# Kernel optimization log

Measured on AMD Instinct MI355X. Metric: run time of the kernel, lower is better.

The kernel has to match this reference:

```python
import jax, jax.numpy as jnp
import numpy as np
from jax import lax

B, S, T = 512, 64, 32
E, H = 512, 1024
VIN, VOUT = 128, 128


def gru_cell(x, h, W_ih, W_hh, b_ih, b_hh):
    # PyTorch GRU cell: gates ordered (r, z, n)
    gi = x @ W_ih.T + b_ih           # [B, 3*Hh]
    gh = h @ W_hh.T + b_hh           # [B, 3*Hh]
    i_r, i_z, i_n = jnp.split(gi, 3, axis=-1)
    h_r, h_z, h_n = jnp.split(gh, 3, axis=-1)
    r = jax.nn.sigmoid(i_r + h_r)
    z = jax.nn.sigmoid(i_z + h_z)
    n = jnp.tanh(i_n + r * h_n)
    return (1.0 - z) * n + z * h


def setup_inputs() -> dict:
    key = jax.random.key(0)
    ks = jax.random.split(key, 18)
    g = lambda k, shp: (jax.random.normal(k, shp, jnp.float32) * 0.05)
    return {
        "src": jax.random.randint(ks[0], (B, S), 0, VIN),
        "tgt": jax.random.randint(ks[1], (B, T), 0, VOUT),
        "enc_emb": g(ks[2], (VIN, E)),
        "dec_emb": g(ks[3], (VOUT, E)),
        "W_ih_f": g(ks[4], (3 * H, E)), "W_hh_f": g(ks[5], (3 * H, H)),
        "b_ih_f": g(ks[6], (3 * H,)), "b_hh_f": g(ks[7], (3 * H,)),
        "W_ih_b": g(ks[8], (3 * H, E)), "W_hh_b": g(ks[9], (3 * H, H)),
        "b_ih_b": g(ks[10], (3 * H,)), "b_hh_b": g(ks[11], (3 * H,)),
        "W_ih_d": g(ks[12], (3 * 2 * H, E)), "W_hh_d": g(ks[13], (3 * 2 * H, 2 * H)),
        "b_ih_d": g(ks[14], (3 * 2 * H,)), "b_hh_d": g(ks[15], (3 * 2 * H,)),
        "W_fc": g(ks[16], (VOUT, 2 * H)), "b_fc": g(ks[17], (VOUT,)),
    }


def reference(src, tgt, enc_emb, dec_emb,
              W_ih_f, W_hh_f, b_ih_f, b_hh_f,
              W_ih_b, W_hh_b, b_ih_b, b_hh_b,
              W_ih_d, W_hh_d, b_ih_d, b_hh_d,
              W_fc, b_fc):
    batch = src.shape[0]
    x = enc_emb[src]                         # [B, S, E]
    x_t = jnp.swapaxes(x, 0, 1)              # [S, B, E]

    def enc_scan(xs, W_ih, W_hh, b_ih, b_hh):
        h0 = jnp.zeros((batch, H), dtype=xs.dtype)
        def step(h, xt):
            h2 = gru_cell(xt, h, W_ih, W_hh, b_ih, b_hh)
            return h2, None
        hT, _ = lax.scan(step, h0, xs)
        return hT                             # final hidden [B, H]

    h_fwd = enc_scan(x_t, W_ih_f, W_hh_f, b_ih_f, b_hh_f)
    h_bwd = enc_scan(x_t[::-1], W_ih_b, W_hh_b, b_ih_b, b_hh_b)
    h = jnp.concatenate([h_fwd, h_bwd], axis=-1)   # [B, 2H] = torch.cat((h[-2], h[-1]), 1)

    tok0 = tgt[:, 0]                          # <sos> tokens

    def dec_step(carry, _):
        hh, tok = carry
        xt = dec_emb[tok]                     # [B, E]
        hh = gru_cell(xt, hh, W_ih_d, W_hh_d, b_ih_d, b_hh_d)
        logits = hh @ W_fc.T + b_fc           # [B, VOUT]
        nxt = jnp.argmax(logits, axis=-1)     # greedy feedback (teacher_forcing_ratio=0)
        return (hh, nxt), logits

    (_, _), logits = lax.scan(dec_step, (h, tok0), None, length=tgt.shape[1] - 1)
    return jnp.swapaxes(logits, 0, 1)         # [B, T-1, VOUT]
```

## Files before the change

kernel.cpp:

```cpp
#include <hip/hip_runtime.h>
#include <math.h>

#define B 512
#define S 64
#define T 32
#define E 512
#define H 1024
#define VOUTD 128
#define H2 (2*H)
#define H3 (3*H)
#define H6 (6*H)

typedef unsigned short ushortT;
typedef unsigned int uintT;
typedef __attribute__((ext_vector_type(8))) short short8;
typedef __attribute__((ext_vector_type(4))) float floatx4;

__device__ __forceinline__ float sigmoidf_(float x) { return 1.0f / (1.0f + expf(-x)); }

__device__ __forceinline__ uintT pack_hi2(float a, float b) {
    return (__float_as_uint(a) >> 16) | (__float_as_uint(b) & 0xFFFF0000u);
}
__device__ __forceinline__ uintT pack_lo2(float a, float b) {
    uintT ua = __float_as_uint(a), ub = __float_as_uint(b);
    uintT la = __float_as_uint(a - __uint_as_float(ua & 0xFFFF0000u)) >> 16;
    uintT lb = __float_as_uint(b - __uint_as_float(ub & 0xFFFF0000u)) >> 16;
    return la | (lb << 16);
}

__global__ __launch_bounds__(256) void zero16(uint4* __restrict__ p, int n)
{
    int i = blockIdx.x * 256 + threadIdx.x;
    if (i < n) p[i] = make_uint4(0u, 0u, 0u, 0u);
}

__global__ __launch_bounds__(256) void swizzle_w(
    const float* __restrict__ W, ushortT* __restrict__ out, int njShift, int kShift)
{
    const int K = 8 << kShift;
    const int nj = 1 << njShift;
    const int ncK = K >> 5;
    const int total = (nj >> 4) * ncK * 3;
    int f = blockIdx.x * 4 + (threadIdx.x >> 6);
    if (f >= total) return;
    const int lane = threadIdx.x & 63;
    int g = f % 3;
    int rest = f / 3;
    int c = rest & (ncK - 1);
    int jb = rest >> (kShift - 2);
    int jl = lane & 15, kq = lane >> 4;
    int row = g * nj + jb * 16 + jl;
    int k = c * 32 + kq * 8;
    const float* s = W + (size_t)row * K + k;
    float4 f0 = *(const float4*)s;
    float4 f1 = *(const float4*)(s + 4);
    uint4 hv = make_uint4(pack_hi2(f0.x, f0.y), pack_hi2(f0.z, f0.w),
                          pack_hi2(f1.x, f1.y), pack_hi2(f1.z, f1.w));
    uint4 lv = make_uint4(pack_lo2(f0.x, f0.y), pack_lo2(f0.z, f0.w),
                          pack_lo2(f1.x, f1.y), pack_lo2(f1.z, f1.w));
    size_t base = (size_t)f * 1024 + (size_t)lane * 8;
    *(uint4*)(out + base) = hv;
    *(uint4*)(out + base + 512) = lv;
}

#define MFMA16(a, b, c) __builtin_amdgcn_mfma_f32_16x16x32_bf16(a, b, c, 0, 0, 0)

#define LOADSET(SET, C)                                                         \
    {                                                                           \
        const ushortT* bp_ = bPtr + (size_t)(C) * 3072;                         \
        SET##b[0] = *(const short8*)(bp_);                                      \
        SET##b[1] = *(const short8*)(bp_ + 512);                                \
        SET##b[2] = *(const short8*)(bp_ + 1024);                               \
        SET##b[3] = *(const short8*)(bp_ + 1536);                               \
        SET##b[4] = *(const short8*)(bp_ + 2048);                               \
        SET##b[5] = *(const short8*)(bp_ + 2560);                               \
        const ushortT* ap_ = aPtr + (size_t)(C) * 1024;                         \
        SET##a[0] = *(const short8*)(ap_);                                      \
        SET##a[1] = *(const short8*)(ap_ + 512);                                \
        SET##a[2] = *(const short8*)(ap_ + NCKd * 1024);                        \
        SET##a[3] = *(const short8*)(ap_ + NCKd * 1024 + 512);                  \
    }

#define COMPSET(SET)                                                            \
    _Pragma("unroll")                                                           \
    for (int g = 0; g < 3; ++g) {                                               \
        short8 bh_ = SET##b[g * 2], bl_ = SET##b[g * 2 + 1];                    \
        acc[0][g] = MFMA16(SET##a[0], bh_, acc[0][g]);                          \
        acc[0][g] = MFMA16(SET##a[0], bl_, acc[0][g]);                          \
        acc[0][g] = MFMA16(SET##a[1], bh_, acc[0][g]);                          \
        acc[1][g] = MFMA16(SET##a[2], bh_, acc[1][g]);                          \
        acc[1][g] = MFMA16(SET##a[2], bl_, acc[1][g]);                          \
        acc[1][g] = MFMA16(SET##a[3], bh_, acc[1][g]);                          \
    }

#define MAIN_LOOP()                                                             \
    LOADSET(s0, 0);                                                             \
    LOADSET(s1, 1);                                                             \
    LOADSET(s2, 2);                                                             \
    for (int c = 0; c < NCKd; c += 4) {                                         \
        LOADSET(s3, c + 3);                                                     \
        COMPSET(s0);                                                            \
        if (c + 4 < NCKd) LOADSET(s0, c + 4);                                   \
        COMPSET(s1);                                                            \
        if (c + 5 < NCKd) LOADSET(s1, c + 5);                                   \
        COMPSET(s2);                                                            \
        if (c + 6 < NCKd) LOADSET(s2, c + 6);                                   \
        COMPSET(s3);                                                            \
    }

#define EPILOGUE_STORE(NCKA)                                                    \
    __syncthreads();                                                            \
    _Pragma("unroll")                                                           \
    for (int v = 0; v < 2; ++v) {                                               \
        int idx = t * 2 + v;                                                    \
        int rbo = idx >> 7;                                                     \
        int offs = (idx & 127) * 8;                                             \
        size_t gbase = ((size_t)((m0 >> 4) + rbo) * (NCKA) + cA) * 1024;        \
        *(uint4*)(AfrOut + gbase + offs) = *(const uint4*)&eb[rbo * 1024 + offs]; \
    }

__global__ __launch_bounds__(256, 2) void fused_step_enc(
    const ushortT* __restrict__ Afr,
    const ushortT* __restrict__ WfrF, const ushortT* __restrict__ WfrB,
    const float* __restrict__ giTabF, const float* __restrict__ giTabB,
    const int* __restrict__ src, int s,
    const float* __restrict__ bhF, const float* __restrict__ bhB,
    float* __restrict__ h, ushortT* __restrict__ AfrOut)
{
    __shared__ ushortT eb[4096];
    const int t = threadIdx.x, lane = t & 63, w = t >> 6;
    const int bid = blockIdx.x;
    const int xcd = bid & 7, q = bid >> 3;
    const int jg = xcd + 8 * (q & 3);
    const int mb = q >> 2;
    const int j0 = jg * 32, m0 = mb * 64;
    const bool bwd = (m0 >= B);
    const ushortT* Wfr = bwd ? WfrB : WfrF;
    const float* giTab = bwd ? giTabB : giTabF;
    const float* bh = bwd ? bhB : bhF;
    const int NCKd = 32;
    const int sidx = bwd ? (S - 1 - s) : s;

    const int wr = w >> 1, wc = w & 1;
    const ushortT* aPtr = Afr + (size_t)((m0 >> 4) + wr * 2) * (NCKd * 1024) + lane * 8;
    const ushortT* bPtr = Wfr + (size_t)(jg * 2 + wc) * (NCKd * 3072) + lane * 8;

    floatx4 acc[2][3];
#pragma unroll
    for (int mi = 0; mi < 2; ++mi)
#pragma unroll
        for (int g = 0; g < 3; ++g) acc[mi][g] = (floatx4){0.f, 0.f, 0.f, 0.f};

    short8 s0b[6], s0a[4], s1b[6], s1a[4], s2b[6], s2a[4], s3b[6], s3a[4];
    MAIN_LOOP();

    const int colj = j0 + wc * 16 + (lane & 15);
    const float bR = bh[colj], bZ = bh[H + colj], bN = bh[2 * H + colj];
    const int rloc0 = wr * 32 + (lane >> 4) * 4;
    const int cA = j0 >> 5;
    const int innerB = ((colj >> 3) & 3) * 128 + (colj & 7);
#pragma unroll
    for (int mi = 0; mi < 2; ++mi) {
#pragma unroll
        for (int r = 0; r < 4; ++r) {
            const int rloc = rloc0 + mi * 16 + r;
            const int row = m0 + rloc;
            const int tk = src[(row & (B - 1)) * S + sidx];
            const float* gi = giTab + (size_t)tk * H3;
            float ghr = acc[mi][0][r] + bR;
            float ghz = acc[mi][1][r] + bZ;
            float ghn = acc[mi][2][r] + bN;
            float rr = sigmoidf_(gi[colj] + ghr);
            float z  = sigmoidf_(gi[H + colj] + ghz);
            float n  = tanhf(gi[2 * H + colj] + rr * ghn);
            const size_t idx = (size_t)row * H + colj;
            float hnew = (1.0f - z) * n + z * h[idx];
            h[idx] = hnew;
            uintT u = __float_as_uint(hnew);
            const int rbl = wr * 2 + mi;
            const int inner = ((lane >> 4) * 4 + r) * 8 + innerB;
            eb[rbl * 1024 + inner] = (ushortT)(u >> 16);
            eb[rbl * 1024 + 512 + inner] =
                (ushortT)(__float_as_uint(hnew - __uint_as_float(u & 0xFFFF0000u)) >> 16);
        }
    }
    EPILOGUE_STORE(32)
}

__global__ __launch_bounds__(256, 2) void fused_step_dec(
    const ushortT* __restrict__ Afr, const ushortT* __restrict__ Wfr,
    const float* __restrict__ giTabD, const int* __restrict__ tok,
    const float* __restrict__ bhD,
    float* __restrict__ h, ushortT* __restrict__ AfrOut)
{
    __shared__ ushortT eb[4096];
    const int t = threadIdx.x, lane = t & 63, w = t >> 6;
    const int bid = blockIdx.x;
    const int xcd = bid & 7, q = bid >> 3;
    const int jg = xcd + 8 * (q & 7);
    const int mb = q >> 3;
    const int j0 = jg * 32, m0 = mb * 64;
    const int NCKd = 64;

    const int wr = w >> 1, wc = w & 1;
    const ushortT* aPtr = Afr + (size_t)((m0 >> 4) + wr * 2) * (NCKd * 1024) + lane * 8;
    const ushortT* bPtr = Wfr + (size_t)(jg * 2 + wc) * (NCKd * 3072) + lane * 8;

    floatx4 acc[2][3];
#pragma unroll
    for (int mi = 0; mi < 2; ++mi)
#pragma unroll
        for (int g = 0; g < 3; ++g) acc[mi][g] = (floatx4){0.f, 0.f, 0.f, 0.f};

    short8 s0b[6], s0a[4], s1b[6], s1a[4], s2b[6], s2a[4], s3b[6], s3a[4];
    MAIN_LOOP();

    const int colj = j0 + wc * 16 + (lane & 15);
    const float bR = bhD[colj], bZ = bhD[H2 + colj], bN = bhD[2 * H2 + colj];
    const int rloc0 = wr * 32 + (lane >> 4) * 4;
    const int cA = j0 >> 5;
    const int innerB = ((colj >> 3) & 3) * 128 + (colj & 7);
#pragma unroll
    for (int mi = 0; mi < 2; ++mi) {
#pragma unroll
        for (int r = 0; r < 4; ++r) {
            const int rloc = rloc0 + mi * 16 + r;
            const int row = m0 + rloc;
            const float* gi = giTabD + (size_t)tok[row] * H6;
            float ghr = acc[mi][0][r] + bR;
            float ghz = acc[mi][1][r] + bZ;
            float ghn = acc[mi][2][r] + bN;
            float rr = sigmoidf_(gi[colj] + ghr);
            float z  = sigmoidf_(gi[H2 + colj] + ghz);
            float n  = tanhf(gi[2 * H2 + colj] + rr * ghn);
            const size_t idx = (size_t)row * H2 + colj;
            float hnew = (1.0f - z) * n + z * h[idx];
            h[idx] = hnew;
            uintT u = __float_as_uint(hnew);
            const int rbl = wr * 2 + mi;
            const int inner = ((lane >> 4) * 4 + r) * 8 + innerB;
            eb[rbl * 1024 + inner] = (ushortT)(u >> 16);
            eb[rbl * 1024 + 512 + inner] =
                (ushortT)(__float_as_uint(hnew - __uint_as_float(u & 0xFFFF0000u)) >> 16);
        }
    }
    EPILOGUE_STORE(64)
}

__global__ __launch_bounds__(256) void init_hh_tok_split(
    const float* __restrict__ h_f, const float* __restrict__ h_b,
    const int* __restrict__ tgt, float* __restrict__ hh,
    ushortT* __restrict__ AfrD, int* __restrict__ tok)
{
    int i = blockIdx.x * blockDim.x + threadIdx.x;
    int b = i >> 11;
    int j = i & 2047;
    float v = (j < H) ? h_f[(size_t)b * H + j] : h_b[(size_t)b * H + (j - H)];
    hh[i] = v;
    uintT u = __float_as_uint(v);
    size_t ao = (((size_t)(b >> 4) * 64 + (j >> 5)) * 2) * 512
              + (size_t)((b & 15) + 16 * ((j >> 3) & 3)) * 8 + (j & 7);
    AfrD[ao] = (ushortT)(u >> 16);
    AfrD[ao + 512] = (ushortT)(__float_as_uint(v - __uint_as_float(u & 0xFFFF0000u)) >> 16);
    if (j == 0) tok[b] = tgt[b * T];
}

__global__ __launch_bounds__(256) void logits_argmax2(
    const float* __restrict__ hh, const float* __restrict__ W_fc,
    const float* __restrict__ b_fc, float* __restrict__ out,
    int* __restrict__ tok, int t)
{
    __shared__ float sh[2][H2];
    __shared__ float sred[2][2][128];
    __shared__ float sval[2][128];
    __shared__ int   sidx[2][128];
    const int tid = threadIdx.x;
    const int col = tid & 127;
    const int kh  = tid >> 7;
    const int b0  = blockIdx.x * 2;

    {
        const float4* srcp = (const float4*)(hh + (size_t)b0 * H2);
        float4* dst = (float4*)sh;
        for (int i = tid; i < 2 * H2 / 4; i += 256) dst[i] = srcp[i];
    }
    __syncthreads();

    const float* wrow = W_fc + (size_t)col * H2 + kh * (H2 / 2);
    const float* s0 = sh[0] + kh * (H2 / 2);
    const float* s1 = sh[1] + kh * (H2 / 2);
    float a0 = 0.f, a1 = 0.f;
#pragma unroll 8
    for (int k = 0; k < H2 / 2; k += 4) {
        float4 w4 = *(const float4*)(wrow + k);
        float4 h0 = *(const float4*)(s0 + k);
        float4 h1 = *(const float4*)(s1 + k);
        a0 += w4.x * h0.x + w4.y * h0.y + w4.z * h0.z + w4.w * h0.w;
        a1 += w4.x * h1.x + w4.y * h1.y + w4.z * h1.z + w4.w * h1.w;
    }
    sred[kh][0][col] = a0;
    sred[kh][1][col] = a1;
    __syncthreads();

    if (kh == 0) {
        float l0 = sred[0][0][col] + sred[1][0][col] + b_fc[col];
        float l1 = sred[0][1][col] + sred[1][1][col] + b_fc[col];
        out[(size_t)(b0 + 0) * ((T - 1) * VOUTD) + (size_t)t * VOUTD + col] = l0;
        out[(size_t)(b0 + 1) * ((T - 1) * VOUTD) + (size_t)t * VOUTD + col] = l1;
        sval[0][col] = l0; sidx[0][col] = col;
        sval[1][col] = l1; sidx[1][col] = col;
    }
    __syncthreads();

    const int r = tid >> 7, c = tid & 127;
    for (int off = 64; off > 0; off >>= 1) {
        if (c < off) {
            float ov = sval[r][c + off]; int oi = sidx[r][c + off];
            if (ov > sval[r][c] || (ov == sval[r][c] && oi < sidx[r][c])) {
                sval[r][c] = ov; sidx[r][c] = oi;
            }
        }
        __syncthreads();
    }
    if (tid < 2) tok[b0 + tid] = sidx[tid][0];
}

__global__ __launch_bounds__(256) void gemm_sk(
    const float* __restrict__ Abase, int lda,
    const float* __restrict__ W, float* __restrict__ Cp, int N, int K, int KS)
{
    __shared__ float As[16][68];
    __shared__ float Ws[16][68];
    const int t = threadIdx.x;
    const int m0 = blockIdx.y * 64, n0 = blockIdx.x * 64;
    const int Kc = K / KS, kb = blockIdx.z * Kc;
    const int lr = t >> 2, lc = (t & 3) << 2;
    const int tx = t & 15, ty = t >> 4;
    const int tn0 = tx << 2, tm0 = ty << 2;
    const float* Aptr = Abase + (size_t)(m0 + lr) * lda + kb;
    const float* Wptr = W + (size_t)(n0 + lr) * K + kb;
    float acc[4][4] = {{0.f}};
    for (int k0 = 0; k0 < Kc; k0 += 16) {
        float4 a4 = *(const float4*)(Aptr + k0 + lc);
        float4 w4 = *(const float4*)(Wptr + k0 + lc);
        __syncthreads();
        As[lc+0][lr] = a4.x; As[lc+1][lr] = a4.y; As[lc+2][lr] = a4.z; As[lc+3][lr] = a4.w;
        Ws[lc+0][lr] = w4.x; Ws[lc+1][lr] = w4.y; Ws[lc+2][lr] = w4.z; Ws[lc+3][lr] = w4.w;
        __syncthreads();
#pragma unroll
        for (int kk = 0; kk < 16; ++kk) {
            float4 av = *(const float4*)&As[kk][tm0];
            float4 wv = *(const float4*)&Ws[kk][tn0];
            float am[4] = {av.x, av.y, av.z, av.w};
            float wn[4] = {wv.x, wv.y, wv.z, wv.w};
#pragma unroll
            for (int i = 0; i < 4; ++i)
#pragma unroll
                for (int j = 0; j < 4; ++j) acc[i][j] += am[i] * wn[j];
        }
    }
    float* Cb = Cp + ((size_t)blockIdx.z * VOUTD + m0 + tm0) * N + n0 + tn0;
#pragma unroll
    for (int i = 0; i < 4; ++i)
        *(float4*)(Cb + (size_t)i * N) = make_float4(acc[i][0], acc[i][1], acc[i][2], acc[i][3]);
}

__global__ __launch_bounds__(256) void gi_combine(
    const float* __restrict__ Cp, const float* __restrict__ bias,
    float* __restrict__ Cout, int N, int KS)
{
    int j = blockIdx.x * 256 + threadIdx.x;
    int v = blockIdx.y;
    float s = 0.f;
    for (int z = 0; z < KS; ++z) s += Cp[((size_t)z * VOUTD + v) * N + j];
    Cout[(size_t)v * N + j] = s + bias[j];
}

__global__ __launch_bounds__(256) void gemm_bias(
    const float* __restrict__ Abase,
    const int* __restrict__ idx, int idxStride, int idxOff, int lda,
    const float* __restrict__ W, const float* __restrict__ bias,
    float* __restrict__ C, int N, int K)
{
    __shared__ float As[16][68];
    __shared__ float Ws[16][68];
    const int t = threadIdx.x;
    const int m0 = blockIdx.y * 64, n0 = blockIdx.x * 64;
    const int lr = t >> 2, lc = (t & 3) << 2;
    const int tx = t & 15, ty = t >> 4;
    const int tn0 = tx << 2, tm0 = ty << 2;
    const int arow = m0 + lr;
    const float* Aptr = idx ? (Abase + (size_t)idx[arow * idxStride + idxOff] * lda)
                            : (Abase + (size_t)arow * lda);
    const float* Wptr = W + (size_t)(n0 + lr) * K;
    float acc[4][4] = {{0.f}};
    for (int k0 = 0; k0 < K; k0 += 16) {
        float4 a4 = *(const float4*)(Aptr + k0 + lc);
        float4 w4 = *(const float4*)(Wptr + k0 + lc);
        __syncthreads();
        As[lc+0][lr] = a4.x; As[lc+1][lr] = a4.y; As[lc+2][lr] = a4.z; As[lc+3][lr] = a4.w;
        Ws[lc+0][lr] = w4.x; Ws[lc+1][lr] = w4.y; Ws[lc+2][lr] = w4.z; Ws[lc+3][lr] = w4.w;
        __syncthreads();
#pragma unroll
        for (int kk = 0; kk < 16; ++kk) {
            float4 av = *(const float4*)&As[kk][tm0];
            float4 wv = *(const float4*)&Ws[kk][tn0];
            float am[4] = {av.x, av.y, av.z, av.w};
            float wn[4] = {wv.x, wv.y, wv.z, wv.w};
#pragma unroll
            for (int i = 0; i < 4; ++i)
#pragma unroll
                for (int j = 0; j < 4; ++j) acc[i][j] += am[i] * wn[j];
        }
    }
    const float b0 = bias[n0+tn0], b1 = bias[n0+tn0+1], b2 = bias[n0+tn0+2], b3 = bias[n0+tn0+3];
#pragma unroll
    for (int i = 0; i < 4; ++i) {
        float4 o = make_float4(acc[i][0]+b0, acc[i][1]+b1, acc[i][2]+b2, acc[i][3]+b3);
        *(float4*)(C + (size_t)(m0 + tm0 + i) * N + n0 + tn0) = o;
    }
}

__global__ __launch_bounds__(256) void gemm_enc(
    const float* __restrict__ Abase, int lda, int K,
    const int* __restrict__ srcIdx, int s,
    const float* __restrict__ W1, const float* __restrict__ bias1,
    const float* __restrict__ W2, const float* __restrict__ bias2,
    float* __restrict__ C, int N)
{
    __shared__ float As[16][68];
    __shared__ float Ws[16][68];
    const int t = threadIdx.x;
    const int m0 = blockIdx.y * 64, n0 = blockIdx.x * 64;
    const bool bwd = (m0 >= B);
    const float* W = bwd ? W2 : W1;
    const float* bias = bwd ? bias2 : bias1;
    const int lr = t >> 2, lc = (t & 3) << 2;
    const int tx = t & 15, ty = t >> 4;
    const int tn0 = tx << 2, tm0 = ty << 2;
    const int arow = m0 + lr;
    const float* Aptr;
    if (srcIdx) {
        int r = arow & (B - 1);
        int sidx = bwd ? (S - 1 - s) : s;
        Aptr = Abase + (size_t)srcIdx[r * S + sidx] * lda;
    } else Aptr = Abase + (size_t)arow * lda;
    const float* Wptr = W + (size_t)(n0 + lr) * K;
    float acc[4][4] = {{0.f}};
    for (int k0 = 0; k0 < K; k0 += 16) {
        float4 a4 = *(const float4*)(Aptr + k0 + lc);
        float4 w4 = *(const float4*)(Wptr + k0 + lc);
        __syncthreads();
        As[lc+0][lr] = a4.x; As[lc+1][lr] = a4.y; As[lc+2][lr] = a4.z; As[lc+3][lr] = a4.w;
        Ws[lc+0][lr] = w4.x; Ws[lc+1][lr] = w4.y; Ws[lc+2][lr] = w4.z; Ws[lc+3][lr] = w4.w;
        __syncthreads();
#pragma unroll
        for (int kk = 0; kk < 16; ++kk) {
            float4 av = *(const float4*)&As[kk][tm0];
            float4 wv = *(const float4*)&Ws[kk][tn0];
            float am[4] = {av.x, av.y, av.z, av.w};
            float wn[4] = {wv.x, wv.y, wv.z, wv.w};
#pragma unroll
            for (int i = 0; i < 4; ++i)
#pragma unroll
                for (int j = 0; j < 4; ++j) acc[i][j] += am[i] * wn[j];
        }
    }
    const float b0 = bias[n0+tn0], b1 = bias[n0+tn0+1], b2 = bias[n0+tn0+2], b3 = bias[n0+tn0+3];
#pragma unroll
    for (int i = 0; i < 4; ++i) {
        float4 o = make_float4(acc[i][0]+b0, acc[i][1]+b1, acc[i][2]+b2, acc[i][3]+b3);
        *(float4*)(C + (size_t)(m0 + tm0 + i) * N + n0 + tn0) = o;
    }
}

__global__ __launch_bounds__(256) void gru_gate(
    const float* __restrict__ gi, const float* __restrict__ gh,
    float* __restrict__ h, int Hd)
{
    int i = blockIdx.x * blockDim.x + threadIdx.x;
    int b = i / Hd, j = i - b * Hd;
    const float* gib = gi + (size_t)b * 3 * Hd;
    const float* ghb = gh + (size_t)b * 3 * Hd;
    float r = sigmoidf_(gib[j] + ghb[j]);
    float z = sigmoidf_(gib[Hd + j] + ghb[Hd + j]);
    float n = tanhf(gib[2 * Hd + j] + r * ghb[2 * Hd + j]);
    h[i] = (1.0f - z) * n + z * h[i];
}

__global__ __launch_bounds__(256) void init_hh_tok(
    const float* __restrict__ h_f, const float* __restrict__ h_b,
    const int* __restrict__ tgt, float* __restrict__ hh, int* __restrict__ tok)
{
    int i = blockIdx.x * blockDim.x + threadIdx.x;
    int b = i >> 11, j = i & 2047;
    hh[i] = (j < H) ? h_f[(size_t)b * H + j] : h_b[(size_t)b * H + (j - H)];
    if (j == 0) tok[b] = tgt[b * T];
}

extern "C" void kernel_launch(void* const* d_in, const int* in_sizes, int n_in,
                              void* d_out, int out_size, void* d_ws, size_t ws_size,
                              hipStream_t stream)
{
    const int*   src     = (const int*)d_in[0];
    const int*   tgt     = (const int*)d_in[1];
    const float* enc_emb = (const float*)d_in[2];
    const float* dec_emb = (const float*)d_in[3];
    const float* W_ih_f  = (const float*)d_in[4];
    const float* W_hh_f  = (const float*)d_in[5];
    const float* b_ih_f  = (const float*)d_in[6];
    const float* b_hh_f  = (const float*)d_in[7];
    const float* W_ih_b  = (const float*)d_in[8];
    const float* W_hh_b  = (const float*)d_in[9];
    const float* b_ih_b  = (const float*)d_in[10];
    const float* b_hh_b  = (const float*)d_in[11];
    const float* W_ih_d  = (const float*)d_in[12];
    const float* W_hh_d  = (const float*)d_in[13];
    const float* b_ih_d  = (const float*)d_in[14];
    const float* b_hh_d  = (const float*)d_in[15];
    const float* W_fc    = (const float*)d_in[16];
    const float* b_fc    = (const float*)d_in[17];
    float* out = (float*)d_out;

    char* base = (char*)d_ws;
    size_t off = 0;
    auto alloc = [&](size_t bytes) { char* p = base + off; off += (bytes + 255) & ~(size_t)255; return p; };

    float*   hE     = (float*)  alloc((size_t)2 * B * H * 4);
    ushortT* AfrEA  = (ushortT*)alloc((size_t)2 * B * H * 2 * 2);
    ushortT* AfrEB  = (ushortT*)alloc((size_t)2 * B * H * 2 * 2);
    float*   hh     = (float*)  alloc((size_t)B * H2 * 4);
    ushortT* AfrDA  = (ushortT*)alloc((size_t)B * H2 * 2 * 2);
    ushortT* AfrDB  = (ushortT*)alloc((size_t)B * H2 * 2 * 2);
    float*   giTabF = (float*)  alloc((size_t)VOUTD * H3 * 4);
    float*   giTabB = (float*)  alloc((size_t)VOUTD * H3 * 4);
    float*   giTabD = (float*)  alloc((size_t)VOUTD * H6 * 4);
    float*   giPart = (float*)  alloc((size_t)4 * VOUTD * H6 * 4);
    ushortT* WfrF   = (ushortT*)alloc((size_t)H3 * H * 2 * 2);
    ushortT* WfrB   = (ushortT*)alloc((size_t)H3 * H * 2 * 2);
    ushortT* WfrD   = (ushortT*)alloc((size_t)H6 * H2 * 2 * 2);
    int*     tok    = (int*)    alloc((size_t)B * 4);
    size_t required = off;

    dim3 blk(256);

    if (ws_size >= required) {
        {
            size_t zbytes = (size_t)2 * B * H * 4 + (size_t)2 * B * H * 4;
            int n16 = (int)(zbytes / 16);
            zero16<<<dim3((n16 + 255) / 256), blk, 0, stream>>>((uint4*)hE, n16);
        }
        {
            int fe = (H / 16) * (H / 32) * 3;
            int fd = (H2 / 16) * (H2 / 32) * 3;
            swizzle_w<<<dim3((fe + 3) / 4), blk, 0, stream>>>(W_hh_f, WfrF, 10, 7);
            swizzle_w<<<dim3((fe + 3) / 4), blk, 0, stream>>>(W_hh_b, WfrB, 10, 7);
            swizzle_w<<<dim3((fd + 3) / 4), blk, 0, stream>>>(W_hh_d, WfrD, 11, 8);
        }

        gemm_sk<<<dim3(H3 / 64, VOUTD / 64, 4), blk, 0, stream>>>(
            enc_emb, E, W_ih_f, giPart, H3, E, 4);
        gi_combine<<<dim3(H3 / 256, VOUTD), blk, 0, stream>>>(giPart, b_ih_f, giTabF, H3, 4);
        gemm_sk<<<dim3(H3 / 64, VOUTD / 64, 4), blk, 0, stream>>>(
            enc_emb, E, W_ih_b, giPart, H3, E, 4);
        gi_combine<<<dim3(H3 / 256, VOUTD), blk, 0, stream>>>(giPart, b_ih_b, giTabB, H3, 4);
        gemm_sk<<<dim3(H6 / 64, VOUTD / 64, 4), blk, 0, stream>>>(
            dec_emb, E, W_ih_d, giPart, H6, E, 4);
        gi_combine<<<dim3(H6 / 256, VOUTD), blk, 0, stream>>>(giPart, b_ih_d, giTabD, H6, 4);

        for (int s = 0; s < S; ++s) {
            const ushortT* inA = (s & 1) ? AfrEB : AfrEA;
            ushortT* outA = (s & 1) ? AfrEA : AfrEB;
            fused_step_enc<<<dim3(512), blk, 0, stream>>>(
                inA, WfrF, WfrB, giTabF, giTabB, src, s, b_hh_f, b_hh_b, hE, outA);
        }

        init_hh_tok_split<<<dim3((B * H2) / 256), blk, 0, stream>>>(
            hE, hE + (size_t)B * H, tgt, hh, AfrDA, tok);

        for (int t = 0; t < T - 1; ++t) {
            const ushortT* inA = (t & 1) ? AfrDB : AfrDA;
            ushortT* outA = (t & 1) ? AfrDA : AfrDB;
            fused_step_dec<<<dim3(512), blk, 0, stream>>>(
                inA, WfrD, giTabD, tok, b_hh_d, hh, outA);
            logits_argmax2<<<dim3(B / 2), blk, 0, stream>>>(hh, W_fc, b_fc, out, tok, t);
        }
    } else {
        {
            size_t zbytes = (size_t)2 * B * H * 4;
            int n16 = (int)(zbytes / 16);
            zero16<<<dim3((n16 + 255) / 256), blk, 0, stream>>>((uint4*)hE, n16);
        }
        float* giE = (float*)WfrF;
        float* ghF = giE + (size_t)2 * B * H3;
        dim3 grid_gi(H3 / 64, (2 * B) / 64);
        dim3 grid_gate((2 * B * H) / 256);
        for (int s = 0; s < S; ++s) {
            gemm_enc<<<grid_gi, blk, 0, stream>>>(enc_emb, E, E, src, s,
                                                  W_ih_f, b_ih_f, W_ih_b, b_ih_b, giE, H3);
            gemm_enc<<<grid_gi, blk, 0, stream>>>(hE, H, H, nullptr, 0,
                                                  W_hh_f, b_hh_f, W_hh_b, b_hh_b, ghF, H3);
            gru_gate<<<grid_gate, blk, 0, stream>>>(giE, ghF, hE, H);
        }
        init_hh_tok<<<dim3((B * H2) / 256), blk, 0, stream>>>(hE, hE + (size_t)B * H, tgt, hh, tok);
        dim3 grid_d(H6 / 64, B / 64);
        dim3 grid_dgate((B * H2) / 256);
        for (int t = 0; t < T - 1; ++t) {
            gemm_bias<<<grid_d, blk, 0, stream>>>(dec_emb, tok, 1, 0, E,
                                                  W_ih_d, b_ih_d, giE, H6, E);
            gemm_bias<<<grid_d, blk, 0, stream>>>(hh, nullptr, 0, 0, H2,
                                                  W_hh_d, b_hh_d, ghF, H6, H2);
            gru_gate<<<grid_dgate, blk, 0, stream>>>(giE, ghF, hh, H2);
            logits_argmax2<<<dim3(B / 2), blk, 0, stream>>>(hh, W_fc, b_fc, out, tok, t);
        }
    }
}
```

Measured before the change: 5.595 ms.

## Retile recurrent GRU step kernels to 256x16 tiles with one B column per block

The fused encoder and decoder step kernels now give each block 256 rows and 16 hidden columns (all three gates) instead of 64x32. Each wave owns 64 rows and shares a single B fragment, so weight-fragment reuse per load goes up, and the grid is halved to 256 blocks. The software pipeline drops from four register sets to two to make room for the larger accumulators, occupancy is set to one block per CU, and the epilogue store layout is reworked to match. The risks are less latency hiding, since there are fewer blocks and a shallower prefetch, and possible register pressure.

```diff
diff --git a/kernel.cpp b/kernel.cpp
--- a/kernel.cpp
+++ b/kernel.cpp
@@ -74,52 +74,52 @@
         SET##b[3] = *(const short8*)(bp_ + 1536);                               \
         SET##b[4] = *(const short8*)(bp_ + 2048);                               \
         SET##b[5] = *(const short8*)(bp_ + 2560);                               \
-        const ushortT* ap_ = aPtr + (size_t)(C) * 1024;                         \
-        SET##a[0] = *(const short8*)(ap_);                                      \
-        SET##a[1] = *(const short8*)(ap_ + 512);                                \
-        SET##a[2] = *(const short8*)(ap_ + NCKd * 1024);                        \
-        SET##a[3] = *(const short8*)(ap_ + NCKd * 1024 + 512);                  \
+        _Pragma("unroll")                                                       \
+        for (int rb_ = 0; rb_ < 4; ++rb_) {                                     \
+            const ushortT* ap_ = aPtr + (size_t)rb_ * (NCKd * 1024)             \
+                                      + (size_t)(C) * 1024;                     \
+            SET##a[rb_ * 2]     = *(const short8*)(ap_);                        \
+            SET##a[rb_ * 2 + 1] = *(const short8*)(ap_ + 512);                  \
+        }                                                                       \
     }
 
 #define COMPSET(SET)                                                            \
     _Pragma("unroll")                                                           \
     for (int g = 0; g < 3; ++g) {                                               \
         short8 bh_ = SET##b[g * 2], bl_ = SET##b[g * 2 + 1];                    \
-        acc[0][g] = MFMA16(SET##a[0], bh_, acc[0][g]);                          \
-        acc[0][g] = MFMA16(SET##a[0], bl_, acc[0][g]);                          \
-        acc[0][g] = MFMA16(SET##a[1], bh_, acc[0][g]);                          \
-        acc[1][g] = MFMA16(SET##a[2], bh_, acc[1][g]);                          \
-        acc[1][g] = MFMA16(SET##a[2], bl_, acc[1][g]);                          \
-        acc[1][g] = MFMA16(SET##a[3], bh_, acc[1][g]);                          \
+        _Pragma("unroll")                                                       \
+        for (int mi = 0; mi < 4; ++mi) {                                        \
+            acc[mi][g] = MFMA16(SET##a[mi * 2], bh_, acc[mi][g]);               \
+            acc[mi][g] = MFMA16(SET##a[mi * 2], bl_, acc[mi][g]);               \
+            acc[mi][g] = MFMA16(SET##a[mi * 2 + 1], bh_, acc[mi][g]);           \
+        }                                                                       \
     }
 
 #define MAIN_LOOP()                                                             \
     LOADSET(s0, 0);                                                             \
-    LOADSET(s1, 1);                                                             \
-    LOADSET(s2, 2);                                                             \
-    for (int c = 0; c < NCKd; c += 4) {                                         \
-        LOADSET(s3, c + 3);                                                     \
+    for (int c = 0; c < NCKd; c += 2) {                                         \
+        LOADSET(s1, c + 1);                                                     \
         COMPSET(s0);                                                            \
-        if (c + 4 < NCKd) LOADSET(s0, c + 4);                                   \
+        if (c + 2 < NCKd) LOADSET(s0, c + 2);                                   \
         COMPSET(s1);                                                            \
-        if (c + 5 < NCKd) LOADSET(s1, c + 5);                                   \
-        COMPSET(s2);                                                            \
-        if (c + 6 < NCKd) LOADSET(s2, c + 6);                                   \
-        COMPSET(s3);                                                            \
     }
 
 #define EPILOGUE_STORE(NCKA)                                                    \
     __syncthreads();                                                            \
-    _Pragma("unroll")                                                           \
-    for (int v = 0; v < 2; ++v) {                                               \
-        int idx = t * 2 + v;                                                    \
-        int rbo = idx >> 7;                                                     \
-        int offs = (idx & 127) * 8;                                             \
-        size_t gbase = ((size_t)((m0 >> 4) + rbo) * (NCKA) + cA) * 1024;        \
-        *(uint4*)(AfrOut + gbase + offs) = *(const uint4*)&eb[rbo * 1024 + offs]; \
-    }
-
-__global__ __launch_bounds__(256, 2) void fused_step_enc(
+    {                                                                           \
+        const int run = t >> 3;                                      \
+        const int rb_ = run >> 1;                                    \
+        const int pl_ = run & 1;                                     \
+        const int sub = t & 7;                                                  \
+        const ushortT* sp = &eb[rb_][pl_ * 256 + sub * 32];                     \
+        ushortT* dp = AfrOut + (((size_t)((m0 >> 4) + rb_)) * (NCKA) + cA) * 1024 \
+                    + pl_ * 512 + kqpar * 256 + sub * 32;                       \
+        _Pragma("unroll")                                                       \
+        for (int v = 0; v < 4; ++v)                                             \
+            *(uint4*)(dp + v * 8) = *(const uint4*)(sp + v * 8);                \
+    }
+
+__global__ __launch_bounds__(256, 1) void fused_step_enc(
     const ushortT* __restrict__ Afr,
     const ushortT* __restrict__ WfrF, const ushortT* __restrict__ WfrB,
     const float* __restrict__ giTabF, const float* __restrict__ giTabB,
@@ -127,13 +127,13 @@
     const float* __restrict__ bhF, const float* __restrict__ bhB,
     float* __restrict__ h, ushortT* __restrict__ AfrOut)
 {
-    __shared__ ushortT eb[4096];
+    __shared__ ushortT eb[16][512];
     const int t = threadIdx.x, lane = t & 63, w = t >> 6;
     const int bid = blockIdx.x;
     const int xcd = bid & 7, q = bid >> 3;
-    const int jg = xcd + 8 * (q & 3);
-    const int mb = q >> 2;
-    const int j0 = jg * 32, m0 = mb * 64;
+    const int jg16 = xcd * 8 + (q & 7);
+    const int mb   = q >> 3;
+    const int j0 = jg16 * 16, m0 = mb * 256;
     const bool bwd = (m0 >= B);
     const ushortT* Wfr = bwd ? WfrB : WfrF;
     const float* giTab = bwd ? giTabB : giTabF;
@@ -141,30 +141,30 @@
     const int NCKd = 32;
     const int sidx = bwd ? (S - 1 - s) : s;
 
-    const int wr = w >> 1, wc = w & 1;
-    const ushortT* aPtr = Afr + (size_t)((m0 >> 4) + wr * 2) * (NCKd * 1024) + lane * 8;
-    const ushortT* bPtr = Wfr + (size_t)(jg * 2 + wc) * (NCKd * 3072) + lane * 8;
-
-    floatx4 acc[2][3];
-#pragma unroll
-    for (int mi = 0; mi < 2; ++mi)
+    const ushortT* aPtr = Afr + (size_t)((m0 >> 4) + w * 4) * (NCKd * 1024) + lane * 8;
+    const ushortT* bPtr = Wfr + (size_t)jg16 * (NCKd * 3072) + lane * 8;
+
+    floatx4 acc[4][3];
+#pragma unroll
+    for (int mi = 0; mi < 4; ++mi)
 #pragma unroll
         for (int g = 0; g < 3; ++g) acc[mi][g] = (floatx4){0.f, 0.f, 0.f, 0.f};
 
-    short8 s0b[6], s0a[4], s1b[6], s1a[4], s2b[6], s2a[4], s3b[6], s3a[4];
+    short8 s0b[6], s0a[8], s1b[6], s1a[8];
     MAIN_LOOP();
 
-    const int colj = j0 + wc * 16 + (lane & 15);
+    const int colj = j0 + (lane & 15);
     const float bR = bh[colj], bZ = bh[H + colj], bN = bh[2 * H + colj];
-    const int rloc0 = wr * 32 + (lane >> 4) * 4;
-    const int cA = j0 >> 5;
-    const int innerB = ((colj >> 3) & 3) * 128 + (colj & 7);
-#pragma unroll
-    for (int mi = 0; mi < 2; ++mi) {
+    const int cA = jg16 >> 1;
+    const int kqpar = jg16 & 1;
+    const int khalf = (lane >> 3) & 1;
+    const int e7 = lane & 7;
+#pragma unroll
+    for (int mi = 0; mi < 4; ++mi) {
 #pragma unroll
         for (int r = 0; r < 4; ++r) {
-            const int rloc = rloc0 + mi * 16 + r;
-            const int row = m0 + rloc;
+            const int r15 = (lane >> 4) * 4 + r;
+            const int row = m0 + w * 64 + mi * 16 + r15;
             const int tk = src[(row & (B - 1)) * S + sidx];
             const float* gi = giTab + (size_t)tk * H3;
             float ghr = acc[mi][0][r] + bR;
@@ -177,55 +177,54 @@
             float hnew = (1.0f - z) * n + z * h[idx];
             h[idx] = hnew;
             uintT u = __float_as_uint(hnew);
-            const int rbl = wr * 2 + mi;
-            const int inner = ((lane >> 4) * 4 + r) * 8 + innerB;
-            eb[rbl * 1024 + inner] = (ushortT)(u >> 16);
-            eb[rbl * 1024 + 512 + inner] =
+            const int slot = (r15 + 16 * khalf) * 8 + e7;
+            eb[w * 4 + mi][slot] = (ushortT)(u >> 16);
+            eb[w * 4 + mi][256 + slot] =
                 (ushortT)(__float_as_uint(hnew - __uint_as_float(u & 0xFFFF0000u)) >> 16);
         }
     }
     EPILOGUE_STORE(32)
 }
 
-__global__ __launch_bounds__(256, 2) void fused_step_dec(
+__global__ __launch_bounds__(256, 1) void fused_step_dec(
     const ushortT* __restrict__ Afr, const ushortT* __restrict__ Wfr,
     const float* __restrict__ giTabD, const int* __restrict__ tok,
     const float* __restrict__ bhD,
     float* __restrict__ h, ushortT* __restrict__ AfrOut)
 {
-    __shared__ ushortT eb[4096];
+    __shared__ ushortT eb[16][512];
     const int t = threadIdx.x, lane = t & 63, w = t >> 6;
     const int bid = blockIdx.x;
     const int xcd = bid & 7, q = bid >> 3;
-    const int jg = xcd + 8 * (q & 7);
-    const int mb = q >> 3;
-    const int j0 = jg * 32, m0 = mb * 64;
+    const int jg16 = xcd * 16 + (q & 15);
+    const int mb   = q >> 4;
+    const int j0 = jg16 * 16, m0 = mb * 256;
     const int NCKd = 64;
 
-    const int wr = w >> 1, wc = w & 1;
-    const ushortT* aPtr = Afr + (size_t)((m0 >> 4) + wr * 2) * (NCKd * 1024) + lane * 8;
-    const ushortT* bPtr = Wfr + (size_t)(jg * 2 + wc) * (NCKd * 3072) + lane * 8;
-
-    floatx4 acc[2][3];
-#pragma unroll
-    for (int mi = 0; mi < 2; ++mi)
+    const ushortT* aPtr = Afr + (size_t)((m0 >> 4) + w * 4) * (NCKd * 1024) + lane * 8;
+    const ushortT* bPtr = Wfr + (size_t)jg16 * (NCKd * 3072) + lane * 8;
+
+    floatx4 acc[4][3];
+#pragma unroll
+    for (int mi = 0; mi < 4; ++mi)
 #pragma unroll
         for (int g = 0; g < 3; ++g) acc[mi][g] = (floatx4){0.f, 0.f, 0.f, 0.f};
 
-    short8 s0b[6], s0a[4], s1b[6], s1a[4], s2b[6], s2a[4], s3b[6], s3a[4];
+    short8 s0b[6], s0a[8], s1b[6], s1a[8];
     MAIN_LOOP();
 
-    const int colj = j0 + wc * 16 + (lane & 15);
+    const int colj = j0 + (lane & 15);
     const float bR = bhD[colj], bZ = bhD[H2 + colj], bN = bhD[2 * H2 + colj];
-    const int rloc0 = wr * 32 + (lane >> 4) * 4;
-    const int cA = j0 >> 5;
-    const int innerB = ((colj >> 3) & 3) * 128 + (colj & 7);
-#pragma unroll
-    for (int mi = 0; mi < 2; ++mi) {
+    const int cA = jg16 >> 1;
+    const int kqpar = jg16 & 1;
+    const int khalf = (lane >> 3) & 1;
+    const int e7 = lane & 7;
+#pragma unroll
+    for (int mi = 0; mi < 4; ++mi) {
 #pragma unroll
         for (int r = 0; r < 4; ++r) {
-            const int rloc = rloc0 + mi * 16 + r;
-            const int row = m0 + rloc;
+            const int r15 = (lane >> 4) * 4 + r;
+            const int row = m0 + w * 64 + mi * 16 + r15;
             const float* gi = giTabD + (size_t)tok[row] * H6;
             float ghr = acc[mi][0][r] + bR;
             float ghz = acc[mi][1][r] + bZ;
@@ -237,10 +236,9 @@
             float hnew = (1.0f - z) * n + z * h[idx];
             h[idx] = hnew;
             uintT u = __float_as_uint(hnew);
-            const int rbl = wr * 2 + mi;
-            const int inner = ((lane >> 4) * 4 + r) * 8 + innerB;
-            eb[rbl * 1024 + inner] = (ushortT)(u >> 16);
-            eb[rbl * 1024 + 512 + inner] =
+            const int slot = (r15 + 16 * khalf) * 8 + e7;
+            eb[w * 4 + mi][slot] = (ushortT)(u >> 16);
+            eb[w * 4 + mi][256 + slot] =
                 (ushortT)(__float_as_uint(hnew - __uint_as_float(u & 0xFFFF0000u)) >> 16);
         }
     }
@@ -571,7 +569,7 @@
         for (int s = 0; s < S; ++s) {
             const ushortT* inA = (s & 1) ? AfrEB : AfrEA;
             ushortT* outA = (s & 1) ? AfrEA : AfrEB;
-            fused_step_enc<<<dim3(512), blk, 0, stream>>>(
+            fused_step_enc<<<dim3(256), blk, 0, stream>>>(
                 inA, WfrF, WfrB, giTabF, giTabB, src, s, b_hh_f, b_hh_b, hE, outA);
         }
 
@@ -581,7 +579,7 @@
         for (int t = 0; t < T - 1; ++t) {
             const ushortT* inA = (t & 1) ? AfrDB : AfrDA;
             ushortT* outA = (t & 1) ? AfrDA : AfrDB;
-            fused_step_dec<<<dim3(512), blk, 0, stream>>>(
+            fused_step_dec<<<dim3(256), blk, 0, stream>>>(
                 inA, WfrD, giTabD, tok, b_hh_d, hh, outA);
             logits_argmax2<<<dim3(B / 2), blk, 0, stream>>>(hh, W_fc, b_fc, out, tok, t);
         }
```

Measured after the change: 4.805 ms. -14.1%, faster.
